# Performance work log

Hardware: AMD Instinct MI355X
Metric: run time of the kernel (lower is better)

## Reference

```python
import jax, jax.numpy as jnp
import numpy as np

B, WIN, D_IN = 512, 512, 128
HID, D_OUT = 256, 64
PLEN = 64


def setup_inputs() -> dict:
    key = jax.random.key(0)
    ks = jax.random.split(key, 10)
    s = 0.05
    return {
        "x": jax.random.normal(ks[0], (B, WIN, D_IN), dtype=jnp.float32),
        "plength": PLEN,
        # AdditiveScore params (torch.randn init)
        "V": jax.random.normal(ks[1], (D_IN, 1), dtype=jnp.float32) * s,
        "W": jax.random.normal(ks[2], (D_IN, 2 * HID), dtype=jnp.float32) * s,
        "U": jax.random.normal(ks[3], (D_IN, D_IN), dtype=jnp.float32) * s,
        # LSTM params, torch gate order [i, f, g, o]
        "W_ih": jax.random.normal(ks[4], (4 * HID, D_IN + D_OUT), dtype=jnp.float32) * s,
        "W_hh": jax.random.normal(ks[5], (4 * HID, HID), dtype=jnp.float32) * s,
        "b_ih": jax.random.normal(ks[6], (4 * HID,), dtype=jnp.float32) * s,
        "b_hh": jax.random.normal(ks[7], (4 * HID,), dtype=jnp.float32) * s,
        # Dense head
        "Wd": jax.random.normal(ks[8], (D_OUT, HID), dtype=jnp.float32) * s,
        "bd": jax.random.normal(ks[9], (D_OUT,), dtype=jnp.float32) * s,
    }


def reference(x, V, W, U, W_ih, W_hh, b_ih, b_hh, Wd, bd, plength):
    b, win, d_in = x.shape
    hid = W_hh.shape[1]
    d_out = Wd.shape[0]
    Uk = jnp.einsum('vd,bwd->bvw', U, x)
    v = V[:, 0]  # (v_d,)

    def step(carry, _):
        s, c, y = carry  # s,c: (b,hid); y: (b,d_out)
        q = jnp.concatenate([s, c], axis=1)          # (b, 2*hid)
        Wq = q @ W.T                                 # (b, v_d)
        # e = V^T tanh(W q + U k), softmax over window
        e = jnp.einsum('v,bvw->bw', v, jnp.tanh(Wq[:, :, None] + Uk))
        w = jax.nn.softmax(e, axis=-1)
        ctx = jnp.einsum('bw,bwd->bd', w, x)         # (b, d_in)
        inp = jnp.concatenate([y, ctx], axis=1)      # (b, d_out + d_in)
        gates = inp @ W_ih.T + s @ W_hh.T + b_ih + b_hh
        i_g, f_g, g_g, o_g = jnp.split(gates, 4, axis=1)
        c_new = jax.nn.sigmoid(f_g) * c + jax.nn.sigmoid(i_g) * jnp.tanh(g_g)
        s_new = jax.nn.sigmoid(o_g) * jnp.tanh(c_new)
        y_new = s_new @ Wd.T + bd                    # (b, d_out)
        return (s_new, c_new, y_new), (y_new, w)

    init = (jnp.zeros((b, hid), x.dtype), jnp.zeros((b, hid), x.dtype),
            jnp.zeros((b, d_out), x.dtype))
    _, (ys, ws) = jax.lax.scan(step, init, None, length=plength)
    predict_y = jnp.transpose(ys, (1, 0, 2))  # (b, plength, d_out)
    weight = jnp.transpose(ws, (1, 0, 2))
    return predict_y, weight
```

## Files before the change

### kernel.cpp

```cpp
#include <hip/hip_runtime.h>
#include <cstdint>
#include <cstddef>

#define BB    512
#define WINN  512
#define DIN   128
#define HIDN  256
#define DOUTN 64
#define PLENN 64
#define G4    1024
#define SCALE2LOG2E 2.88539008177793f
#define XS    0.0416666666667f

typedef short bf16x8 __attribute__((ext_vector_type(8)));
typedef float f32x4 __attribute__((ext_vector_type(4)));

__device__ __forceinline__ float tanh_fast(float xx) {
  float e = __expf(2.0f * xx);
  return 1.0f - 2.0f * __builtin_amdgcn_rcpf(e + 1.0f);
}
__device__ __forceinline__ float sigmoid_fast(float xx) {
  return __builtin_amdgcn_rcpf(1.0f + __expf(-xx));
}
__device__ __forceinline__ ushort f2bf(float f) {
  uint32_t u = __float_as_uint(f);
  return (ushort)((u + 0x7fffu + ((u >> 16) & 1u)) >> 16);
}
__device__ __forceinline__ float bflo(uint32_t u) { return __uint_as_float(u << 16); }
__device__ __forceinline__ float bfhi(uint32_t u) { return __uint_as_float(u & 0xffff0000u); }
__device__ __forceinline__ float ub(uint32_t raw, int byte) {
  return (float)((raw >> (byte * 8)) & 255u);
}
__device__ __forceinline__ uint32_t q8(float v, float sc) {
  float qf = fminf(fmaxf(fmaf(v, sc, 128.5f), 0.f), 255.f);
  return (uint32_t)(int)qf;
}
__device__ __forceinline__ float sterm(uint32_t raw, int byte, float tq, float mv, float acc) {
  float qf = ub(raw, byte);
  return fmaf(mv, __builtin_amdgcn_rcpf(
                    __builtin_amdgcn_exp2f(fmaf(qf, 0.0625f, tq)) + 1.f), acc);
}

__global__ void prep_weights(const float* __restrict__ W, const float* __restrict__ W_ih,
                             const float* __restrict__ W_hh, const float* __restrict__ b_ih,
                             const float* __restrict__ b_hh, const float* __restrict__ Wd,
                             const float* __restrict__ V, const float* __restrict__ U,
                             float* __restrict__ A32, ushort* __restrict__ WihT16,
                             float* __restrict__ Wdt, float* __restrict__ bias,
                             float* __restrict__ m2vv,
                             ushort* __restrict__ Uh16, ushort* __restrict__ Ul16)
{
  int i = blockIdx.x * 256 + threadIdx.x;
  if (i < 512 * 192) {
    int k = i / 192, r = i - k * 192;
    float val;
    if (r < 128) val = SCALE2LOG2E * W[r * 512 + k];
    else         val = (k < 256) ? Wd[(r - 128) * 256 + k] : 0.f;
    A32[i] = val;
  }
  if (i < 448 * 1024) {
    int k = i >> 10, g = i & 1023;
    float v = (k < 192) ? W_ih[g * 192 + k] : W_hh[g * 256 + (k - 192)];
    WihT16[i] = f2bf(v);
  }
  if (i < 256 * 64) { int h = i >> 6, d = i & 63; Wdt[i] = Wd[d * 256 + h]; }
  if (i < 1024) bias[i] = b_ih[i] + b_hh[i];
  if (i < 128) m2vv[i] = -2.0f * V[i];
  if (i < 128 * 128) {
    float us = SCALE2LOG2E * U[i];
    ushort h = f2bf(us);
    float lo = us - __uint_as_float((uint32_t)h << 16);
    Uh16[i] = h;
    Ul16[i] = f2bf(lo);
  }
}

__global__ __launch_bounds__(256) void convert_x(const float* __restrict__ x,
                                                 ushort* __restrict__ x16,
                                                 unsigned char* __restrict__ x8q)
{
  size_t i = ((size_t)blockIdx.x * 256 + threadIdx.x) * 8;
  float4 a = *(const float4*)(x + i);
  float4 b = *(const float4*)(x + i + 4);
  uint4 o;
  o.x = (uint32_t)f2bf(a.x) | ((uint32_t)f2bf(a.y) << 16);
  o.y = (uint32_t)f2bf(a.z) | ((uint32_t)f2bf(a.w) << 16);
  o.z = (uint32_t)f2bf(b.x) | ((uint32_t)f2bf(b.y) << 16);
  o.w = (uint32_t)f2bf(b.z) | ((uint32_t)f2bf(b.w) << 16);
  *(uint4*)(x16 + i) = o;
  uint2 p;
  p.x = q8(a.x, 24.f) | (q8(a.y, 24.f) << 8) | (q8(a.z, 24.f) << 16) | (q8(a.w, 24.f) << 24);
  p.y = q8(b.x, 24.f) | (q8(b.y, 24.f) << 8) | (q8(b.z, 24.f) << 16) | (q8(b.w, 24.f) << 24);
  *(uint2*)(x8q + i) = p;
}

__global__ __launch_bounds__(256) void compute_uk_mfma(const ushort* __restrict__ x16,
                                                       const ushort* __restrict__ Uh16,
                                                       const ushort* __restrict__ Ul16,
                                                       unsigned char* __restrict__ UkT8)
{
  int bidx = blockIdx.x;
  int b   = bidx >> 3;
  int sub = bidx & 7;
  int vs  = sub >> 2;
  int wsb = sub & 3;
  int tid = threadIdx.x;
  int wave = tid >> 6;
  int lane = tid & 63;
  int lr = lane & 15;
  int lk = lane >> 4;

  int v_base = vs * 64 + wave * 16;
  int w_blk  = wsb * 128;

  bf16x8 ah[4], al[4];
#pragma unroll
  for (int kt = 0; kt < 4; ++kt) {
    ah[kt] = *(const bf16x8*)(Uh16 + (size_t)(v_base + lr) * 128 + kt * 32 + lk * 8);
    al[kt] = *(const bf16x8*)(Ul16 + (size_t)(v_base + lr) * 128 + kt * 32 + lk * 8);
  }

#pragma unroll 2
  for (int wt = 0; wt < 8; ++wt) {
    int w0 = w_blk + wt * 16;
    f32x4 acc = {0.f, 0.f, 0.f, 0.f};
#pragma unroll
    for (int kt = 0; kt < 4; ++kt) {
      const ushort* pb = x16 + ((size_t)b * 512 + w0 + lr) * 128 + kt * 32 + lk * 8;
      bf16x8 bv = *(const bf16x8*)pb;
      acc = __builtin_amdgcn_mfma_f32_16x16x32_bf16(ah[kt], bv, acc, 0, 0, 0);
      acc = __builtin_amdgcn_mfma_f32_16x16x32_bf16(al[kt], bv, acc, 0, 0, 0);
    }
    uint32_t q = q8(acc[0], 16.f) | (q8(acc[1], 16.f) << 8) |
                 (q8(acc[2], 16.f) << 16) | (q8(acc[3], 16.f) << 24);
    *(uint32_t*)(UkT8 + ((size_t)b * 512 + w0 + lr) * 128 + v_base + lk * 4) = q;
  }
}

__global__ __launch_bounds__(512) void lstm_qy(const float* __restrict__ g0,
    const float* __restrict__ g1, const float* __restrict__ c_in,
    float* __restrict__ c_out, float* __restrict__ s, float* __restrict__ ybuf,
    const float* __restrict__ A32, const float* __restrict__ bd,
    float* __restrict__ tqs_g, float* __restrict__ outy, int t)
{
  __shared__ float q_lds[8][512];
  int tid = threadIdx.x;
  int b0 = blockIdx.x * 8;
  int strip = blockIdx.y;

  if (t > 0) {
#pragma unroll
    for (int rep = 0; rep < 4; ++rep) {
      int cell = tid + rep * 512;
      int bl = cell >> 8, h = cell & 255;
      int b = b0 + bl;
      size_t gb = (size_t)b * 1024;
      float gi = g0[gb + h]       + g1[gb + h];
      float gf = g0[gb + 256 + h] + g1[gb + 256 + h];
      float gg = g0[gb + 512 + h] + g1[gb + 512 + h];
      float go = g0[gb + 768 + h] + g1[gb + 768 + h];
      float cv = c_in[b * 256 + h];
      float cn = sigmoid_fast(gf) * cv + sigmoid_fast(gi) * tanh_fast(gg);
      float sn = sigmoid_fast(go) * tanh_fast(cn);
      q_lds[bl][h] = sn;
      q_lds[bl][256 + h] = cn;
      if (strip == 0) { c_out[b * 256 + h] = cn; s[b * 256 + h] = sn; }
    }
  } else {
#pragma unroll
    for (int rep = 0; rep < 4; ++rep) {
      int cell = tid + rep * 512;
      int bl = cell >> 8, h = cell & 255;
      q_lds[bl][h] = 0.f; q_lds[bl][256 + h] = 0.f;
    }
  }
  __syncthreads();

  int r = strip * 64 + (tid & 63);
  int tb = tid >> 6;
  int b = b0 + tb;
  float acc0 = (r < 128) ? -8.0f : bd[r - 128];
  float acc1 = 0.f;
  const float* ap = A32 + r;
  const float* qp = &q_lds[tb][0];
#pragma unroll 8
  for (int k = 0; k < 512; k += 2) {
    acc0 = fmaf(ap[(size_t)k * 192], qp[k], acc0);
    acc1 = fmaf(ap[(size_t)(k + 1) * 192], qp[k + 1], acc1);
  }
  float acc = acc0 + acc1;
  if (r < 128) {
    tqs_g[b * 128 + r] = acc;
  } else if (t > 0) {
    int d = r - 128;
    ybuf[b * 64 + d] = acc;
    outy[(size_t)b * PLENN * 64 + (size_t)(t - 1) * 64 + d] = acc;
  }
}

__global__ __launch_bounds__(512, 4) void attn_stream(const unsigned char* __restrict__ UkT8,
    const unsigned char* __restrict__ x8q, const float* __restrict__ tqs_g,
    const float* __restrict__ m2vv_g, float* __restrict__ ctx,
    float* __restrict__ wout, int t)
{
  __shared__ float tqs[128];
  __shared__ float m2vv[128];
  __shared__ float e_sh[512];
  __shared__ float watt[512];
  __shared__ float red[16];
  __shared__ float cp2[544];
  __shared__ float scratch[4096];
  int tid = threadIdx.x;
  int b = blockIdx.x;

  if (tid < 128) tqs[tid] = tqs_g[b * 128 + tid];
  else if (tid < 256) m2vv[tid - 128] = m2vv_g[tid - 128];
  __syncthreads();

  {
    int vs = tid & 7, wg = tid >> 3;
    float tq[16], mv[16];
#pragma unroll
    for (int q4 = 0; q4 < 4; ++q4) {
      float4 t4 = *(const float4*)&tqs[vs * 16 + q4 * 4];
      float4 m4 = *(const float4*)&m2vv[vs * 16 + q4 * 4];
      tq[q4 * 4 + 0] = t4.x; tq[q4 * 4 + 1] = t4.y; tq[q4 * 4 + 2] = t4.z; tq[q4 * 4 + 3] = t4.w;
      mv[q4 * 4 + 0] = m4.x; mv[q4 * 4 + 1] = m4.y; mv[q4 * 4 + 2] = m4.z; mv[q4 * 4 + 3] = m4.w;
    }
    float a8[8];
#pragma unroll
    for (int wi = 0; wi < 8; ++wi) {
      int w = wg + wi * 64;
      uint4 r0 = *(const uint4*)(UkT8 + ((size_t)b * 512 + w) * 128 + vs * 16);
      float a = 0.f;
      a = sterm(r0.x, 0, tq[ 0], mv[ 0], a);
      a = sterm(r0.x, 1, tq[ 1], mv[ 1], a);
      a = sterm(r0.x, 2, tq[ 2], mv[ 2], a);
      a = sterm(r0.x, 3, tq[ 3], mv[ 3], a);
      a = sterm(r0.y, 0, tq[ 4], mv[ 4], a);
      a = sterm(r0.y, 1, tq[ 5], mv[ 5], a);
      a = sterm(r0.y, 2, tq[ 6], mv[ 6], a);
      a = sterm(r0.y, 3, tq[ 7], mv[ 7], a);
      a = sterm(r0.z, 0, tq[ 8], mv[ 8], a);
      a = sterm(r0.z, 1, tq[ 9], mv[ 9], a);
      a = sterm(r0.z, 2, tq[10], mv[10], a);
      a = sterm(r0.z, 3, tq[11], mv[11], a);
      a = sterm(r0.w, 0, tq[12], mv[12], a);
      a = sterm(r0.w, 1, tq[13], mv[13], a);
      a = sterm(r0.w, 2, tq[14], mv[14], a);
      a = sterm(r0.w, 3, tq[15], mv[15], a);
      a8[wi] = a;
    }
#pragma unroll
    for (int wi = 0; wi < 8; ++wi) {
      a8[wi] += __shfl_xor(a8[wi], 1);
      a8[wi] += __shfl_xor(a8[wi], 2);
      a8[wi] += __shfl_xor(a8[wi], 4);
    }
    if (vs == 0) {
#pragma unroll
      for (int wi = 0; wi < 8; ++wi) e_sh[wg + wi * 64] = a8[wi];
    }
  }
  __syncthreads();

  float e = e_sh[tid];
  float m = e;
#pragma unroll
  for (int o = 32; o > 0; o >>= 1) m = fmaxf(m, __shfl_xor(m, o));
  if ((tid & 63) == 0) red[tid >> 6] = m;
  __syncthreads();
  float M = red[0];
#pragma unroll
  for (int i2 = 1; i2 < 8; ++i2) M = fmaxf(M, red[i2]);
  float p = __expf(e - M);
  float wsum = p;
#pragma unroll
  for (int o = 32; o > 0; o >>= 1) wsum += __shfl_xor(wsum, o);
  if ((tid & 63) == 0) red[8 + (tid >> 6)] = wsum;
  __syncthreads();
  float S = red[8] + red[9] + red[10] + red[11] + red[12] + red[13] + red[14] + red[15];
  float wv = p * __builtin_amdgcn_rcpf(S);
  watt[tid] = wv;
  wout[(size_t)b * PLENN * 512 + (size_t)t * 512 + tid] = wv;
  __syncthreads();

  {
    int dg = tid & 15, wch = tid >> 4;
    float a8[8];
#pragma unroll
    for (int i = 0; i < 8; ++i) a8[i] = 0.f;
    const unsigned char* xp = x8q + ((size_t)(b * 512 + wch * 16)) * 128 + dg * 8;
#pragma unroll 4
    for (int wi = 0; wi < 16; ++wi) {
      uint2 raw = *(const uint2*)(xp + (size_t)wi * 128);
      float wgt = watt[wch * 16 + wi];
      a8[0] = fmaf(wgt, ub(raw.x, 0), a8[0]);
      a8[1] = fmaf(wgt, ub(raw.x, 1), a8[1]);
      a8[2] = fmaf(wgt, ub(raw.x, 2), a8[2]);
      a8[3] = fmaf(wgt, ub(raw.x, 3), a8[3]);
      a8[4] = fmaf(wgt, ub(raw.y, 0), a8[4]);
      a8[5] = fmaf(wgt, ub(raw.y, 1), a8[5]);
      a8[6] = fmaf(wgt, ub(raw.y, 2), a8[6]);
      a8[7] = fmaf(wgt, ub(raw.y, 3), a8[7]);
    }
    int rot = (dg + wch) & 7;
    int sbase = wch * 128 + dg * 8;
#pragma unroll
    for (int i = 0; i < 8; ++i) scratch[sbase + ((i + rot) & 7)] = a8[i];
  }
  __syncthreads();
  {
    int p2 = tid >> 7, d = tid & 127;
    float a = 0.f;
#pragma unroll
    for (int k = 0; k < 8; ++k) {
      int wch = p2 * 8 + k;
      a += scratch[wch * 128 + (d & ~7) + (((d & 7) + (d >> 3) + wch) & 7)];
    }
    cp2[p2 * 136 + d] = a;
  }
  __syncthreads();
  if (tid < 128) {
    float a = cp2[tid] + cp2[136 + tid] + cp2[272 + tid] + cp2[408 + tid];
    ctx[b * 128 + tid] = fmaf(a, XS, -128.0f * XS);
  }
}

__global__ __launch_bounds__(256) void gates_gemm(const float* __restrict__ y,
    const float* __restrict__ ctx, const float* __restrict__ s,
    const ushort* __restrict__ WihT16, const float* __restrict__ bias,
    float* __restrict__ g0, float* __restrict__ g1)
{
  __shared__ float As[32][36];
  __shared__ float Bs[32][68];
  int tid = threadIdx.x;
  int bm = blockIdx.x;
  int bn = blockIdx.y;
  int kz = blockIdx.z;
  int tr = tid & 15, tc = tid >> 4;
  float acc[2][4];
#pragma unroll
  for (int i = 0; i < 2; ++i)
#pragma unroll
    for (int j = 0; j < 4; ++j) acc[i][j] = 0.f;

  for (int kt = 0; kt < 7; ++kt) {
    int k0 = kz * 224 + kt * 32;
    const float* Ab; int stride, off;
    if (k0 < 64)       { Ab = y;   stride = 64;  off = 0; }
    else if (k0 < 192) { Ab = ctx; stride = 128; off = 64; }
    else               { Ab = s;   stride = 256; off = 192; }
#pragma unroll
    for (int i = 0; i < 4; ++i) {
      int idx = tid + i * 256;
      int r = idx >> 5, kk = idx & 31;
      As[kk][r] = Ab[(size_t)(bm * 32 + r) * stride + (k0 - off) + kk];
    }
#pragma unroll
    for (int i = 0; i < 4; ++i) {
      int idx = tid + i * 256;
      int kk = idx >> 5, cp = idx & 31;
      uint32_t w2 = *(const uint32_t*)(WihT16 + (size_t)(k0 + kk) * 1024 + bn * 64 + cp * 2);
      Bs[kk][cp * 2]     = bflo(w2);
      Bs[kk][cp * 2 + 1] = bfhi(w2);
    }
    __syncthreads();
#pragma unroll 8
    for (int kk = 0; kk < 32; ++kk) {
      float2 a2 = *(const float2*)&As[kk][tr * 2];
      float4 b4 = *(const float4*)&Bs[kk][tc * 4];
      acc[0][0] = fmaf(a2.x, b4.x, acc[0][0]);
      acc[0][1] = fmaf(a2.x, b4.y, acc[0][1]);
      acc[0][2] = fmaf(a2.x, b4.z, acc[0][2]);
      acc[0][3] = fmaf(a2.x, b4.w, acc[0][3]);
      acc[1][0] = fmaf(a2.y, b4.x, acc[1][0]);
      acc[1][1] = fmaf(a2.y, b4.y, acc[1][1]);
      acc[1][2] = fmaf(a2.y, b4.z, acc[1][2]);
      acc[1][3] = fmaf(a2.y, b4.w, acc[1][3]);
    }
    __syncthreads();
  }
  float* dst = kz ? g1 : g0;
#pragma unroll
  for (int i = 0; i < 2; ++i) {
    int bb = bm * 32 + tr * 2 + i;
    int g  = bn * 64 + tc * 4;
    float4 o4;
    o4.x = acc[i][0] + (kz == 0 ? bias[g + 0] : 0.f);
    o4.y = acc[i][1] + (kz == 0 ? bias[g + 1] : 0.f);
    o4.z = acc[i][2] + (kz == 0 ? bias[g + 2] : 0.f);
    o4.w = acc[i][3] + (kz == 0 ? bias[g + 3] : 0.f);
    *(float4*)(dst + (size_t)bb * 1024 + g) = o4;
  }
}

__global__ __launch_bounds__(256) void lstm_tail(const float* __restrict__ g0,
    const float* __restrict__ g1, const float* __restrict__ c_in,
    const float* __restrict__ Wdt, const float* __restrict__ bd,
    float* __restrict__ outy, int t)
{
  __shared__ float ssh[256];
  int b = blockIdx.x, h = threadIdx.x;
  size_t gb = (size_t)b * 1024;
  float gi = g0[gb + h]       + g1[gb + h];
  float gf = g0[gb + 256 + h] + g1[gb + 256 + h];
  float gg = g0[gb + 512 + h] + g1[gb + 512 + h];
  float go = g0[gb + 768 + h] + g1[gb + 768 + h];
  float cv = c_in[b * 256 + h];
  float cn = sigmoid_fast(gf) * cv + sigmoid_fast(gi) * tanh_fast(gg);
  float sn = sigmoid_fast(go) * tanh_fast(cn);
  ssh[h] = sn;
  __syncthreads();
  if (h < 64) {
    float a = bd[h];
#pragma unroll 4
    for (int k = 0; k < 256; ++k) a = fmaf(ssh[k], Wdt[k * 64 + h], a);
    outy[(size_t)b * PLENN * 64 + (size_t)t * 64 + h] = a;
  }
}

extern "C" void kernel_launch(void* const* d_in, const int* in_sizes, int n_in,
                              void* d_out, int out_size, void* d_ws, size_t ws_size,
                              hipStream_t stream)
{
  (void)in_sizes; (void)n_in; (void)out_size; (void)ws_size;
  const float* x    = (const float*)d_in[0];
  const float* V    = (const float*)d_in[2];
  const float* W    = (const float*)d_in[3];
  const float* U    = (const float*)d_in[4];
  const float* W_ih = (const float*)d_in[5];
  const float* W_hh = (const float*)d_in[6];
  const float* b_ih = (const float*)d_in[7];
  const float* b_hh = (const float*)d_in[8];
  const float* Wd   = (const float*)d_in[9];
  const float* bd   = (const float*)d_in[10];

  float* out  = (float*)d_out;
  float* outy = out;
  float* outw = out + (size_t)BB * PLENN * DOUTN;

  float* ws = (float*)d_ws;
  size_t o = 0;
  unsigned char* UkT8 = (unsigned char*)(ws + o); o += (size_t)BB * DIN * WINN / 4;
  unsigned char* x8q  = (unsigned char*)(ws + o); o += (size_t)BB * WINN * DIN / 4;
  ushort* x16  = (ushort*)(ws + o); o += (size_t)BB * WINN * DIN / 2;
  float* A32  = ws + o; o += 512 * 192;
  ushort* WihT16 = (ushort*)(ws + o); o += 448 * 1024 / 2;
  float* Wdt  = ws + o; o += 256 * 64;
  float* bias = ws + o; o += 1024;
  float* m2vv = ws + o; o += 128;
  ushort* Uh16 = (ushort*)(ws + o); o += 128 * 128 / 2;
  ushort* Ul16 = (ushort*)(ws + o); o += 128 * 128 / 2;
  float* sbuf = ws + o; o += (size_t)BB * HIDN;
  float* cbuf = ws + o; o += (size_t)2 * BB * HIDN;
  float* ybuf = ws + o; o += (size_t)BB * DOUTN;
  float* ctx  = ws + o; o += (size_t)BB * DIN;
  float* tqs_g = ws + o; o += (size_t)BB * DIN;
  float* g0   = ws + o; o += (size_t)BB * G4;
  float* g1   = ws + o; o += (size_t)BB * G4;

  hipMemsetAsync(sbuf, 0, (size_t)BB * HIDN * sizeof(float), stream);
  hipMemsetAsync(cbuf, 0, (size_t)2 * BB * HIDN * sizeof(float), stream);
  hipMemsetAsync(ybuf, 0, (size_t)BB * DOUTN * sizeof(float), stream);

  prep_weights<<<1792, 256, 0, stream>>>(W, W_ih, W_hh, b_ih, b_hh, Wd, V, U,
                                         A32, WihT16, Wdt, bias, m2vv, Uh16, Ul16);
  convert_x<<<16384, 256, 0, stream>>>(x, x16, x8q);
  compute_uk_mfma<<<4096, 256, 0, stream>>>(x16, Uh16, Ul16, UkT8);

  for (int t = 0; t < PLENN; ++t) {
    const float* cin = cbuf + (size_t)((t + 1) & 1) * BB * HIDN;
    float* cout      = cbuf + (size_t)(t & 1) * BB * HIDN;
    lstm_qy<<<dim3(64, 3), 512, 0, stream>>>(g0, g1, cin, cout, sbuf, ybuf,
                                             A32, bd, tqs_g, outy, t);
    attn_stream<<<BB, 512, 0, stream>>>(UkT8, x8q, tqs_g, m2vv, ctx, outw, t);
    gates_gemm<<<dim3(16, 16, 2), 256, 0, stream>>>(ybuf, ctx, sbuf, WihT16, bias, g0, g1);
  }
  lstm_tail<<<BB, 256, 0, stream>>>(g0, g1, cbuf + (size_t)BB * HIDN,
                                    Wdt, bd, outy, PLENN - 1);
}
```

Before: 3.140 ms.

## Split LSTM cell from q/y GEMM and hoist global loads in attention and Uk kernels

The fused lstm_qy kernel, which recomputed the LSTM cell update in each of its 3 strips, is split into lstm_s (one pass over cells, writing c, s and a concatenated q buffer) and qy_gemm (reads q from global memory). The c buffer is updated in place instead of ping-ponged, and the memsets for s and c are dropped because t=0 now zeroes them. attn_stream now issues all UkT8 and x8q loads up front to expose more memory-level parallelism. compute_uk_mfma preloads its B fragments and uses two independent MFMA accumulators. In exchange this adds one kernel launch per timestep and raises register pressure.

```diff
diff --git a/kernel.cpp b/kernel.cpp
--- a/kernel.cpp
+++ b/kernel.cpp
@@ -120,69 +120,64 @@
     al[kt] = *(const bf16x8*)(Ul16 + (size_t)(v_base + lr) * 128 + kt * 32 + lk * 8);
   }
 
-#pragma unroll 2
+#pragma unroll
   for (int wt = 0; wt < 8; ++wt) {
     int w0 = w_blk + wt * 16;
-    f32x4 acc = {0.f, 0.f, 0.f, 0.f};
+    bf16x8 bv[4];
+#pragma unroll
+    for (int kt = 0; kt < 4; ++kt)
+      bv[kt] = *(const bf16x8*)(x16 + ((size_t)b * 512 + w0 + lr) * 128 + kt * 32 + lk * 8);
+    f32x4 acch = {0.f, 0.f, 0.f, 0.f};
+    f32x4 accl = {0.f, 0.f, 0.f, 0.f};
 #pragma unroll
     for (int kt = 0; kt < 4; ++kt) {
-      const ushort* pb = x16 + ((size_t)b * 512 + w0 + lr) * 128 + kt * 32 + lk * 8;
-      bf16x8 bv = *(const bf16x8*)pb;
-      acc = __builtin_amdgcn_mfma_f32_16x16x32_bf16(ah[kt], bv, acc, 0, 0, 0);
-      acc = __builtin_amdgcn_mfma_f32_16x16x32_bf16(al[kt], bv, acc, 0, 0, 0);
-    }
+      acch = __builtin_amdgcn_mfma_f32_16x16x32_bf16(ah[kt], bv[kt], acch, 0, 0, 0);
+      accl = __builtin_amdgcn_mfma_f32_16x16x32_bf16(al[kt], bv[kt], accl, 0, 0, 0);
+    }
+    f32x4 acc = acch + accl;
     uint32_t q = q8(acc[0], 16.f) | (q8(acc[1], 16.f) << 8) |
                  (q8(acc[2], 16.f) << 16) | (q8(acc[3], 16.f) << 24);
     *(uint32_t*)(UkT8 + ((size_t)b * 512 + w0 + lr) * 128 + v_base + lk * 4) = q;
   }
 }
 
-__global__ __launch_bounds__(512) void lstm_qy(const float* __restrict__ g0,
-    const float* __restrict__ g1, const float* __restrict__ c_in,
-    float* __restrict__ c_out, float* __restrict__ s, float* __restrict__ ybuf,
+__global__ __launch_bounds__(256) void lstm_s(const float* __restrict__ g0,
+    const float* __restrict__ g1, float* __restrict__ c, float* __restrict__ s,
+    float* __restrict__ qcat, int t)
+{
+  int b = blockIdx.x, h = threadIdx.x;
+  if (t > 0) {
+    size_t gb = (size_t)b * 1024;
+    float gi = g0[gb + h]       + g1[gb + h];
+    float gf = g0[gb + 256 + h] + g1[gb + 256 + h];
+    float gg = g0[gb + 512 + h] + g1[gb + 512 + h];
+    float go = g0[gb + 768 + h] + g1[gb + 768 + h];
+    float cv = c[b * 256 + h];
+    float cn = sigmoid_fast(gf) * cv + sigmoid_fast(gi) * tanh_fast(gg);
+    float sn = sigmoid_fast(go) * tanh_fast(cn);
+    c[b * 256 + h] = cn;
+    s[b * 256 + h] = sn;
+    qcat[(size_t)b * 512 + h] = sn;
+    qcat[(size_t)b * 512 + 256 + h] = cn;
+  } else {
+    c[b * 256 + h] = 0.f;
+    s[b * 256 + h] = 0.f;
+    qcat[(size_t)b * 512 + h] = 0.f;
+    qcat[(size_t)b * 512 + 256 + h] = 0.f;
+  }
+}
+
+__global__ __launch_bounds__(512) void qy_gemm(const float* __restrict__ qcat,
     const float* __restrict__ A32, const float* __restrict__ bd,
-    float* __restrict__ tqs_g, float* __restrict__ outy, int t)
-{
-  __shared__ float q_lds[8][512];
+    float* __restrict__ tqs_g, float* __restrict__ ybuf, float* __restrict__ outy, int t)
+{
   int tid = threadIdx.x;
-  int b0 = blockIdx.x * 8;
-  int strip = blockIdx.y;
-
-  if (t > 0) {
-#pragma unroll
-    for (int rep = 0; rep < 4; ++rep) {
-      int cell = tid + rep * 512;
-      int bl = cell >> 8, h = cell & 255;
-      int b = b0 + bl;
-      size_t gb = (size_t)b * 1024;
-      float gi = g0[gb + h]       + g1[gb + h];
-      float gf = g0[gb + 256 + h] + g1[gb + 256 + h];
-      float gg = g0[gb + 512 + h] + g1[gb + 512 + h];
-      float go = g0[gb + 768 + h] + g1[gb + 768 + h];
-      float cv = c_in[b * 256 + h];
-      float cn = sigmoid_fast(gf) * cv + sigmoid_fast(gi) * tanh_fast(gg);
-      float sn = sigmoid_fast(go) * tanh_fast(cn);
-      q_lds[bl][h] = sn;
-      q_lds[bl][256 + h] = cn;
-      if (strip == 0) { c_out[b * 256 + h] = cn; s[b * 256 + h] = sn; }
-    }
-  } else {
-#pragma unroll
-    for (int rep = 0; rep < 4; ++rep) {
-      int cell = tid + rep * 512;
-      int bl = cell >> 8, h = cell & 255;
-      q_lds[bl][h] = 0.f; q_lds[bl][256 + h] = 0.f;
-    }
-  }
-  __syncthreads();
-
-  int r = strip * 64 + (tid & 63);
-  int tb = tid >> 6;
-  int b = b0 + tb;
+  int b = blockIdx.x * 8 + (tid >> 6);
+  int r = blockIdx.y * 64 + (tid & 63);
+  const float* qp = qcat + (size_t)b * 512;
+  const float* ap = A32 + r;
   float acc0 = (r < 128) ? -8.0f : bd[r - 128];
   float acc1 = 0.f;
-  const float* ap = A32 + r;
-  const float* qp = &q_lds[tb][0];
 #pragma unroll 8
   for (int k = 0; k < 512; k += 2) {
     acc0 = fmaf(ap[(size_t)k * 192], qp[k], acc0);
@@ -219,6 +214,10 @@
 
   {
     int vs = tid & 7, wg = tid >> 3;
+    uint4 rr[8];
+#pragma unroll
+    for (int wi = 0; wi < 8; ++wi)
+      rr[wi] = *(const uint4*)(UkT8 + ((size_t)b * 512 + wg + wi * 64) * 128 + vs * 16);
     float tq[16], mv[16];
 #pragma unroll
     for (int q4 = 0; q4 < 4; ++q4) {
@@ -230,8 +229,7 @@
     float a8[8];
 #pragma unroll
     for (int wi = 0; wi < 8; ++wi) {
-      int w = wg + wi * 64;
-      uint4 r0 = *(const uint4*)(UkT8 + ((size_t)b * 512 + w) * 128 + vs * 16);
+      uint4 r0 = rr[wi];
       float a = 0.f;
       a = sterm(r0.x, 0, tq[ 0], mv[ 0], a);
       a = sterm(r0.x, 1, tq[ 1], mv[ 1], a);
@@ -287,22 +285,32 @@
 
   {
     int dg = tid & 15, wch = tid >> 4;
+    const unsigned char* xp = x8q + ((size_t)(b * 512 + wch * 16)) * 128 + dg * 8;
+    uint2 raw[16];
+#pragma unroll
+    for (int wi = 0; wi < 16; ++wi)
+      raw[wi] = *(const uint2*)(xp + (size_t)wi * 128);
+    float wgt[16];
+#pragma unroll
+    for (int q4 = 0; q4 < 4; ++q4) {
+      float4 w4 = *(const float4*)&watt[wch * 16 + q4 * 4];
+      wgt[q4 * 4 + 0] = w4.x; wgt[q4 * 4 + 1] = w4.y;
+      wgt[q4 * 4 + 2] = w4.z; wgt[q4 * 4 + 3] = w4.w;
+    }
     float a8[8];
 #pragma unroll
     for (int i = 0; i < 8; ++i) a8[i] = 0.f;
-    const unsigned char* xp = x8q + ((size_t)(b * 512 + wch * 16)) * 128 + dg * 8;
-#pragma unroll 4
+#pragma unroll
     for (int wi = 0; wi < 16; ++wi) {
-      uint2 raw = *(const uint2*)(xp + (size_t)wi * 128);
-      float wgt = watt[wch * 16 + wi];
-      a8[0] = fmaf(wgt, ub(raw.x, 0), a8[0]);
-      a8[1] = fmaf(wgt, ub(raw.x, 1), a8[1]);
-      a8[2] = fmaf(wgt, ub(raw.x, 2), a8[2]);
-      a8[3] = fmaf(wgt, ub(raw.x, 3), a8[3]);
-      a8[4] = fmaf(wgt, ub(raw.y, 0), a8[4]);
-      a8[5] = fmaf(wgt, ub(raw.y, 1), a8[5]);
-      a8[6] = fmaf(wgt, ub(raw.y, 2), a8[6]);
-      a8[7] = fmaf(wgt, ub(raw.y, 3), a8[7]);
+      float wg2 = wgt[wi];
+      a8[0] = fmaf(wg2, ub(raw[wi].x, 0), a8[0]);
+      a8[1] = fmaf(wg2, ub(raw[wi].x, 1), a8[1]);
+      a8[2] = fmaf(wg2, ub(raw[wi].x, 2), a8[2]);
+      a8[3] = fmaf(wg2, ub(raw[wi].x, 3), a8[3]);
+      a8[4] = fmaf(wg2, ub(raw[wi].y, 0), a8[4]);
+      a8[5] = fmaf(wg2, ub(raw[wi].y, 1), a8[5]);
+      a8[6] = fmaf(wg2, ub(raw[wi].y, 2), a8[6]);
+      a8[7] = fmaf(wg2, ub(raw[wi].y, 3), a8[7]);
     }
     int rot = (dg + wch) & 7;
     int sbase = wch * 128 + dg * 8;
@@ -453,15 +461,14 @@
   ushort* Uh16 = (ushort*)(ws + o); o += 128 * 128 / 2;
   ushort* Ul16 = (ushort*)(ws + o); o += 128 * 128 / 2;
   float* sbuf = ws + o; o += (size_t)BB * HIDN;
-  float* cbuf = ws + o; o += (size_t)2 * BB * HIDN;
+  float* cbuf = ws + o; o += (size_t)BB * HIDN;
+  float* qcat = ws + o; o += (size_t)BB * 512;
   float* ybuf = ws + o; o += (size_t)BB * DOUTN;
   float* ctx  = ws + o; o += (size_t)BB * DIN;
   float* tqs_g = ws + o; o += (size_t)BB * DIN;
   float* g0   = ws + o; o += (size_t)BB * G4;
   float* g1   = ws + o; o += (size_t)BB * G4;
 
-  hipMemsetAsync(sbuf, 0, (size_t)BB * HIDN * sizeof(float), stream);
-  hipMemsetAsync(cbuf, 0, (size_t)2 * BB * HIDN * sizeof(float), stream);
   hipMemsetAsync(ybuf, 0, (size_t)BB * DOUTN * sizeof(float), stream);
 
   prep_weights<<<1792, 256, 0, stream>>>(W, W_ih, W_hh, b_ih, b_hh, Wd, V, U,
@@ -470,13 +477,10 @@
   compute_uk_mfma<<<4096, 256, 0, stream>>>(x16, Uh16, Ul16, UkT8);
 
   for (int t = 0; t < PLENN; ++t) {
-    const float* cin = cbuf + (size_t)((t + 1) & 1) * BB * HIDN;
-    float* cout      = cbuf + (size_t)(t & 1) * BB * HIDN;
-    lstm_qy<<<dim3(64, 3), 512, 0, stream>>>(g0, g1, cin, cout, sbuf, ybuf,
-                                             A32, bd, tqs_g, outy, t);
+    lstm_s<<<BB, 256, 0, stream>>>(g0, g1, cbuf, sbuf, qcat, t);
+    qy_gemm<<<dim3(64, 3), 512, 0, stream>>>(qcat, A32, bd, tqs_g, ybuf, outy, t);
     attn_stream<<<BB, 512, 0, stream>>>(UkT8, x8q, tqs_g, m2vv, ctx, outw, t);
     gates_gemm<<<dim3(16, 16, 2), 256, 0, stream>>>(ybuf, ctx, sbuf, WihT16, bias, g0, g1);
   }
-  lstm_tail<<<BB, 256, 0, stream>>>(g0, g1, cbuf + (size_t)BB * HIDN,
-                                    Wdt, bd, outy, PLENN - 1);
-}
+  lstm_tail<<<BB, 256, 0, stream>>>(g0, g1, cbuf, Wdt, bd, outy, PLENN - 1);
+}
```

Result: slower. 3.414 ms (+8.7%).
